# Kernel tuning notes

Measured on AMD Instinct MI355X. Metric: run time of the kernel, lower is better.

## Reference

```python
import jax, jax.numpy as jnp
import numpy as np

NUM_POS_FEATS = 512
LEN_EMBEDDING = 64


def setup_inputs() -> dict:
    key = jax.random.key(0)
    k1, k2 = jax.random.split(key)
    x = jax.random.normal(k1, (32, 3, 64, 64), dtype=jnp.float32)
    # nn.init.uniform_ -> U[0,1)
    row_embed = jax.random.uniform(k2, (LEN_EMBEDDING, NUM_POS_FEATS), dtype=jnp.float32)
    return {"x": x, "row_embed": row_embed}


def reference(x, row_embed):
    b = x.shape[0]
    h, w = x.shape[-2], x.shape[-1]
    center_x, center_y = w // 2, h // 2
    ii = jnp.arange(h)[:, None]   # row index i
    jj = jnp.arange(w)[None, :]   # col index j
    # shortest-path matrix: max(|cx - j| + |cy - i| - 1, 0)
    Z = jnp.maximum(jnp.abs(center_x - jj) + jnp.abs(center_y - ii) - 1, 0)  # [h, w] int
    pos = row_embed[Z]                          # [h, w, F] single fused gather
    pos = jnp.transpose(pos, (2, 0, 1))         # [F, h, w]
    pos = jnp.broadcast_to(pos[None], (b,) + pos.shape)  # [b, F, h, w]
    return pos
```

## Files before the change

kernel.cpp:

```cpp
#include <hip/hip_runtime.h>
#include <hip/hip_bf16.h>


#define NUM_POS_FEATS 512
#define LEN_EMB 64
#define H 64
#define W 64
#define B 32

__global__ __launch_bounds__(256) void pe_kernel(const float* __restrict__ row_embed,
                                                 float* __restrict__ out) {
    const int t = blockIdx.x * blockDim.x + threadIdx.x;
    const int f   = t >> 10;
    const int rem = t & 1023;
    const int i   = rem >> 4;
    const int j4  = (rem & 15) << 2;

    const int di = abs(32 - i);

    float vals[4];
#pragma unroll
    for (int k = 0; k < 4; ++k) {
        const int j = j4 + k;
        int z = di + abs(32 - j) - 1;
        z = z < 0 ? 0 : z;
        vals[k] = row_embed[z * NUM_POS_FEATS + f];
    }
    const float4 v = make_float4(vals[0], vals[1], vals[2], vals[3]);

    const size_t base    = (size_t)f * (H * W) + (size_t)i * W + (size_t)j4;
    const size_t bstride = (size_t)NUM_POS_FEATS * H * W;

#pragma unroll
    for (int b = 0; b < B; ++b) {
        *reinterpret_cast<float4*>(out + base + (size_t)b * bstride) = v;
    }
}

extern "C" void kernel_launch(void* const* d_in, const int* in_sizes, int n_in,
                              void* d_out, int out_size, void* d_ws, size_t ws_size,
                              hipStream_t stream) {
    const float* row_embed = (const float*)d_in[1];
    float* out = (float*)d_out;

    const int total_quads = NUM_POS_FEATS * H * W / 4;
    const int block = 256;
    const int grid = total_quads / block;
    pe_kernel<<<grid, block, 0, stream>>>(row_embed, out);
}
```

Baseline: 265.6 us.

## Launch one block per batch-feature plane and stage embedding column in LDS

Each block now handles one (batch, feature) output plane of 64x64 floats, so every block writes a contiguous 16 KB region instead of each thread scattering 32 stores across batches. The block first loads the 64 embedding values for its feature into shared memory, then each thread gathers four values per iteration from there. This replaces the strided global gathers with a tiny LDS table but repeats the computation and LDS loads for every batch, and adds a block barrier.

```diff
diff --git a/kernel.cpp b/kernel.cpp
--- a/kernel.cpp
+++ b/kernel.cpp
@@ -3,37 +3,46 @@
 
 
 #define NUM_POS_FEATS 512
-#define LEN_EMB 64
 #define H 64
 #define W 64
 #define B 32
 
 __global__ __launch_bounds__(256) void pe_kernel(const float* __restrict__ row_embed,
                                                  float* __restrict__ out) {
-    const int t = blockIdx.x * blockDim.x + threadIdx.x;
-    const int f   = t >> 10;
-    const int rem = t & 1023;
-    const int i   = rem >> 4;
-    const int j4  = (rem & 15) << 2;
+    __shared__ float col[64];
 
-    const int di = abs(32 - i);
+    const int bf  = blockIdx.x;
+    const int f   = bf & (NUM_POS_FEATS - 1);
+    const int tid = threadIdx.x;
 
-    float vals[4];
+    if (tid < 64) {
+        col[tid] = row_embed[tid * NUM_POS_FEATS + f];
+    }
+    __syncthreads();
+
+    float4* o = reinterpret_cast<float4*>(out + (size_t)bf * (H * W));
+
 #pragma unroll
     for (int k = 0; k < 4; ++k) {
-        const int j = j4 + k;
-        int z = di + abs(32 - j) - 1;
-        z = z < 0 ? 0 : z;
-        vals[k] = row_embed[z * NUM_POS_FEATS + f];
-    }
-    const float4 v = make_float4(vals[0], vals[1], vals[2], vals[3]);
+        const int idx = k * 256 + tid;
+        const int i   = idx >> 4;
+        const int j4  = (idx & 15) << 2;
+        const int di  = abs(32 - i);
 
-    const size_t base    = (size_t)f * (H * W) + (size_t)i * W + (size_t)j4;
-    const size_t bstride = (size_t)NUM_POS_FEATS * H * W;
-
-#pragma unroll
-    for (int b = 0; b < B; ++b) {
-        *reinterpret_cast<float4*>(out + base + (size_t)b * bstride) = v;
+        float4 v;
+        {
+            int z = di + abs(32 - (j4 + 0)) - 1; v.x = col[z < 0 ? 0 : z];
+        }
+        {
+            int z = di + abs(32 - (j4 + 1)) - 1; v.y = col[z < 0 ? 0 : z];
+        }
+        {
+            int z = di + abs(32 - (j4 + 2)) - 1; v.z = col[z < 0 ? 0 : z];
+        }
+        {
+            int z = di + abs(32 - (j4 + 3)) - 1; v.w = col[z < 0 ? 0 : z];
+        }
+        o[idx] = v;
     }
 }
 
@@ -43,8 +52,6 @@
     const float* row_embed = (const float*)d_in[1];
     float* out = (float*)d_out;
 
-    const int total_quads = NUM_POS_FEATS * H * W / 4;
-    const int block = 256;
-    const int grid = total_quads / block;
-    pe_kernel<<<grid, block, 0, stream>>>(row_embed, out);
+    const int grid = B * NUM_POS_FEATS;
+    pe_kernel<<<grid, 256, 0, stream>>>(row_embed, out);
 }
```

New measurement: 256.6 us. 1.04x faster.
